# Optimization experiments

Measured on AMD Instinct MI355X. Metric: run time of the kernel, lower is better.

The kernel has to match this reference:

```python
import jax, jax.numpy as jnp
import numpy as np

B, N, DIM = 64, 197, 768
NUM_HEAD, HEAD_DIM = 12, 64
SCALE = HEAD_DIM ** -0.5
WS = (14, 14)
NUM_REL = (2 * WS[0] - 1) * (2 * WS[1] - 1) + 3  # 732


def _relative_position_index():
    coords = np.stack(np.meshgrid(np.arange(WS[0]), np.arange(WS[1]), indexing='ij'))  # (2, Wh, Ww)
    cf = coords.reshape(2, -1)                              # (2, Wh*Ww)
    rel = (cf[:, :, None] - cf[:, None, :]).transpose(1, 2, 0).astype(np.int64)
    rel[:, :, 0] += WS[0] - 1
    rel[:, :, 1] += WS[1] - 1
    rel[:, :, 0] *= 2 * WS[1] - 1
    idx = np.zeros((WS[0] * WS[1] + 1,) * 2, dtype=np.int32)
    idx[1:, 1:] = rel.sum(-1)
    idx[0, :] = NUM_REL - 3
    idx[:, 0] = NUM_REL - 2
    idx[0, 0] = NUM_REL - 1
    return idx


def setup_inputs() -> dict:
    key = jax.random.key(0)
    k1, k2, k3, k4 = jax.random.split(key, 4)
    x = jax.random.normal(k1, (B, N, DIM), dtype=jnp.float32)
    qkv_w = jax.random.normal(k2, (3 * DIM, DIM), dtype=jnp.float32) * (DIM ** -0.5)
    q_bias = jnp.zeros((DIM,), dtype=jnp.float32)
    v_bias = jnp.zeros((DIM,), dtype=jnp.float32)
    rpb_table = jax.random.normal(k3, (NUM_REL, NUM_HEAD), dtype=jnp.float32) * 0.02
    proj_w = jax.random.normal(k4, (DIM, DIM), dtype=jnp.float32) * (DIM ** -0.5)
    proj_b = jnp.zeros((DIM,), dtype=jnp.float32)
    rel_index = jnp.asarray(_relative_position_index())
    return {"x": x, "qkv_w": qkv_w, "q_bias": q_bias, "v_bias": v_bias,
            "rpb_table": rpb_table, "proj_w": proj_w, "proj_b": proj_b,
            "rel_index": rel_index}


def reference(x, qkv_w, q_bias, v_bias, rpb_table, proj_w, proj_b, rel_index):
    b, n, c = x.shape
    # qkv projection with [q_bias, 0, v_bias] bias layout
    qkv_bias = jnp.concatenate([q_bias, jnp.zeros_like(v_bias), v_bias])
    qkv = x @ qkv_w.T + qkv_bias                               # (B, N, 3*C)
    qkv = qkv.reshape(b, n, 3, NUM_HEAD, HEAD_DIM).transpose(2, 0, 3, 1, 4)
    q, k, v = qkv[0] * SCALE, qkv[1], qkv[2]                   # (B, H, N, hd)
    attn = jnp.einsum('bhqd,bhkd->bhqk', q, k)                 # (B, H, N, N)
    # relative position bias gather: table[(N,N)] -> (N, N, H) -> (H, N, N)
    bias = rpb_table[rel_index].transpose(2, 0, 1)
    attn = jax.nn.softmax(attn + bias[None], axis=-1)
    out = jnp.einsum('bhqk,bhkd->bhqd', attn, v)               # (B, H, N, hd)
    out = out.transpose(0, 2, 1, 3).reshape(b, n, -1)
    return out @ proj_w.T + proj_b
```

## Files before the change

### kernel.cpp

```cpp
#include <hip/hip_runtime.h>


#define B_    64
#define N_    197
#define DIM_  768
#define H_    12
#define HD_   64
#define M_TOT (B_ * N_)

#define OFF_Q   0
#define OFF_K   14976
#define OFF_VT  29952
#define ST_A0   44800
#define ST_A1   51456
#define ST_B0   58112
#define ST_B1   64256
#define OFF_P   44800
#define LDS_TOT 74496

typedef __attribute__((ext_vector_type(8))) short bf8;
typedef __attribute__((ext_vector_type(4))) float f4;

__device__ __forceinline__ unsigned short f2bf(float f) {
    unsigned u = __float_as_uint(f);
    u = (u + 0x7fffu + ((u >> 16) & 1u)) >> 16;
    return (unsigned short)u;
}

__device__ __forceinline__ void gl2lds16(const unsigned short* g, unsigned short* l) {
    __builtin_amdgcn_global_load_lds(
        (const __attribute__((address_space(1))) void*)g,
        (__attribute__((address_space(3))) void*)l, 16, 0, 0);
}

__global__ void k_prep(const float* __restrict__ x, const float* __restrict__ qkvw,
                       const float* __restrict__ projw, const float* __restrict__ rpb,
                       const int* __restrict__ relidx,
                       unsigned short* __restrict__ x_bf, unsigned short* __restrict__ qkvw_bf,
                       unsigned short* __restrict__ projw_bf, float* __restrict__ bias_hqk) {
    const int T = gridDim.x * blockDim.x;
    const int tid = blockIdx.x * blockDim.x + threadIdx.x;
    for (int i = tid; i < M_TOT * DIM_; i += T) x_bf[i] = f2bf(x[i]);
    for (int i = tid; i < 3 * DIM_ * DIM_; i += T) qkvw_bf[i] = f2bf(qkvw[i]);
    for (int i = tid; i < DIM_ * DIM_; i += T) projw_bf[i] = f2bf(projw[i]);
    for (int i = tid; i < H_ * N_ * N_; i += T) {
        int h = i / (N_ * N_), qk = i - h * (N_ * N_);
        bias_hqk[i] = rpb[relidx[qk] * H_ + h];
    }
}

__global__ __launch_bounds__(512, 1) void k_fused(const unsigned short* __restrict__ X,
                                                  const unsigned short* __restrict__ Wqkv,
                                                  const float* __restrict__ qb,
                                                  const float* __restrict__ vbias,
                                                  const float* __restrict__ bias_hqk,
                                                  unsigned short* __restrict__ att_ws) {
    __shared__ unsigned short lds[LDS_TOT];

    const int t = threadIdx.x;
    const int w = t >> 6, lane = t & 63, ln = lane & 15, quad = lane >> 4;
    const int wm = w & 3, wn = w >> 2;
    const int srl = lane >> 3;
    const int src8 = (lane & 7) ^ srl;

    const int gid = blockIdx.x;
    const int local = gid >> 3;
    const int b = (gid & 7) * 8 + (local & 7);
    const int h = local >> 3;

    const unsigned short* xb = X + (size_t)b * 197 * 768;

    auto stage = [&](int kt, int aOfs, int bOfs) {
#pragma unroll
        for (int i = 0; i < 4; ++i) {
            int idx = w + 8 * i;
            if (idx >= 25) break;
            if (idx < 13) {
                int tok = 2 * (idx * 8 + srl) + (src8 >> 2);
                if (tok > 196) tok = 196;
                gl2lds16(xb + (size_t)tok * 768 + kt * 32 + (src8 & 3) * 8,
                         &lds[aOfs + idx * 512]);
            } else {
                int bb = idx - 13;
                int rr = 2 * (bb * 8 + srl) + (src8 >> 2);
                gl2lds16(Wqkv + (size_t)((rr >> 6) * 768 + h * 64 + (rr & 63)) * 768
                              + kt * 32 + (src8 & 3) * 8,
                         &lds[bOfs + bb * 512]);
            }
        }
    };

    f4 acc[3][4][2] = {};

    auto compute = [&](int aOfs, int bOfs) {
        bf8 bfr[3][2];
#pragma unroll
        for (int p = 0; p < 3; ++p)
#pragma unroll
            for (int j2 = 0; j2 < 2; ++j2) {
                int rr = p * 64 + (wn * 2 + j2) * 16 + ln;
                int sr = rr >> 1;
                int slot = (((rr & 1) << 2) | quad) ^ (sr & 7);
                bfr[p][j2] = *(const bf8*)&lds[bOfs + sr * 64 + slot * 8];
            }
#pragma unroll
        for (int mi = 0; mi < 4; ++mi) {
            int mt = wm + 4 * mi;
            if (mt >= 13) continue;
            int row = mt * 16 + ln;
            int sr = row >> 1;
            int slot = (((row & 1) << 2) | quad) ^ (sr & 7);
            bf8 af = *(const bf8*)&lds[aOfs + sr * 64 + slot * 8];
#pragma unroll
            for (int p = 0; p < 3; ++p)
#pragma unroll
                for (int j2 = 0; j2 < 2; ++j2)
                    acc[p][mi][j2] = __builtin_amdgcn_mfma_f32_16x16x32_bf16(
                        af, bfr[p][j2], acc[p][mi][j2], 0, 0, 0);
        }
    };

    stage(0, ST_A0, ST_B0);
    for (int kt2 = 0; kt2 < 24; kt2 += 2) {
        __syncthreads();
        if (kt2 + 1 < 24) stage(kt2 + 1, ST_A1, ST_B1);
        compute(ST_A0, ST_B0);
        __syncthreads();
        if (kt2 + 2 < 24) stage(kt2 + 2, ST_A0, ST_B0);
        if (kt2 + 1 < 24) compute(ST_A1, ST_B1);
    }

#pragma unroll
    for (int p = 0; p < 3; ++p) {
        float bj[2];
#pragma unroll
        for (int j2 = 0; j2 < 2; ++j2) {
            int d = h * 64 + (wn * 2 + j2) * 16 + ln;
            bj[j2] = (p == 0) ? qb[d] : (p == 2) ? vbias[d] : 0.0f;
        }
#pragma unroll
        for (int mi = 0; mi < 4; ++mi) {
            int mt = wm + 4 * mi;
            if (mt >= 13) continue;
#pragma unroll
            for (int j2 = 0; j2 < 2; ++j2) {
                int col = (wn * 2 + j2) * 16 + ln;
#pragma unroll
                for (int r = 0; r < 4; ++r) {
                    int row = mt * 16 + quad * 4 + r;
                    float v = acc[p][mi][j2][r];
                    if (p == 0)      lds[OFF_Q + row * 72 + col] = f2bf((v + bj[j2]) * 0.125f);
                    else if (p == 1) lds[OFF_K + row * 72 + col] = f2bf(v);
                    else             lds[OFF_VT + col * 232 + row] = f2bf(v + bj[j2]);
                }
            }
        }
    }
    __syncthreads();

    for (int idx = t; idx < 64 * 16; idx += 512) {
        int row = idx >> 4, c = 208 + (idx & 15);
        lds[OFF_VT + row * 232 + c] = 0;
    }
    __syncthreads();

    const float* bp = bias_hqk + h * 197 * 197;
    unsigned short* psl = &lds[OFF_P + w * 3712];

    for (int mt = w; mt < 13; mt += 8) {
        bf8 qa[2];
#pragma unroll
        for (int ks = 0; ks < 2; ++ks)
            qa[ks] = *(const bf8*)&lds[OFF_Q + (mt * 16 + ln) * 72 + ks * 32 + quad * 8];

        f4 sacc[13];
#pragma unroll
        for (int nt = 0; nt < 13; ++nt) sacc[nt] = (f4){0.f, 0.f, 0.f, 0.f};
#pragma unroll
        for (int nt = 0; nt < 13; ++nt) {
#pragma unroll
            for (int ks = 0; ks < 2; ++ks) {
                bf8 kb = *(const bf8*)&lds[OFF_K + (nt * 16 + ln) * 72 + ks * 32 + quad * 8];
                sacc[nt] = __builtin_amdgcn_mfma_f32_16x16x32_bf16(qa[ks], kb, sacc[nt], 0, 0, 0);
            }
        }

        int qi[4];
#pragma unroll
        for (int r = 0; r < 4; ++r) { int q0 = mt * 16 + quad * 4 + r; qi[r] = q0 < 197 ? q0 : 196; }
        float mx[4] = {-3.0e38f, -3.0e38f, -3.0e38f, -3.0e38f};
#pragma unroll
        for (int nt = 0; nt < 13; ++nt) {
            int kidx = nt * 16 + ln;
#pragma unroll
            for (int r = 0; r < 4; ++r) {
                float s = (kidx < 197) ? (sacc[nt][r] + bp[qi[r] * 197 + kidx]) : -3.0e38f;
                sacc[nt][r] = s;
                mx[r] = fmaxf(mx[r], s);
            }
        }
#pragma unroll
        for (int r = 0; r < 4; ++r)
#pragma unroll
            for (int off = 1; off < 16; off <<= 1)
                mx[r] = fmaxf(mx[r], __shfl_xor(mx[r], off, 64));

        float sum[4] = {0.f, 0.f, 0.f, 0.f};
#pragma unroll
        for (int nt = 0; nt < 13; ++nt)
#pragma unroll
            for (int r = 0; r < 4; ++r) {
                float pv = __expf(sacc[nt][r] - mx[r]);
                sacc[nt][r] = pv;
                sum[r] += pv;
            }
#pragma unroll
        for (int r = 0; r < 4; ++r)
#pragma unroll
            for (int off = 1; off < 16; off <<= 1)
                sum[r] += __shfl_xor(sum[r], off, 64);
        float inv[4];
#pragma unroll
        for (int r = 0; r < 4; ++r) inv[r] = 1.0f / sum[r];

#pragma unroll
        for (int nt = 0; nt < 13; ++nt)
#pragma unroll
            for (int r = 0; r < 4; ++r)
                psl[(quad * 4 + r) * 232 + nt * 16 + ln] = f2bf(sacc[nt][r] * inv[r]);
        for (int i = lane; i < 256; i += 64)
            psl[(i >> 4) * 232 + 208 + (i & 15)] = 0;
        __asm__ __volatile__("s_waitcnt lgkmcnt(0)" ::: "memory");

        bf8 pa[7];
#pragma unroll
        for (int ks = 0; ks < 7; ++ks)
            pa[ks] = *(const bf8*)&psl[ln * 232 + ks * 32 + quad * 8];
#pragma unroll
        for (int j = 0; j < 4; ++j) {
            f4 o = (f4){0.f, 0.f, 0.f, 0.f};
#pragma unroll
            for (int ks = 0; ks < 7; ++ks) {
                bf8 vf = *(const bf8*)&lds[OFF_VT + (j * 16 + ln) * 232 + ks * 32 + quad * 8];
                o = __builtin_amdgcn_mfma_f32_16x16x32_bf16(pa[ks], vf, o, 0, 0, 0);
            }
#pragma unroll
            for (int r = 0; r < 4; ++r) {
                int tok = mt * 16 + quad * 4 + r;
                if (tok < 197)
                    att_ws[((size_t)b * 197 + tok) * 768 + h * 64 + j * 16 + ln] = f2bf(o[r]);
            }
        }
        __asm__ __volatile__("s_waitcnt lgkmcnt(0)" ::: "memory");
    }
}

__device__ __forceinline__ void pj_stage(const unsigned short* __restrict__ A,
                                         const unsigned short* __restrict__ Bm,
                                         int bm, int bn, int kt, int w, int rsub, int src8,
                                         unsigned short* a_l, unsigned short* b_l) {
#pragma unroll
    for (int c = 0; c < 4; ++c) {
        int rb = w * 32 + c * 8;
        int gr = bm * 128 + rb + rsub;
        if (gr > M_TOT - 1) gr = M_TOT - 1;
        gl2lds16(A + (size_t)gr * 768 + kt * 64 + (src8 << 3), &a_l[rb * 64]);
        int gc = bn * 128 + rb + rsub;
        gl2lds16(Bm + (size_t)gc * 768 + kt * 64 + (src8 << 3), &b_l[rb * 64]);
    }
}

__device__ __forceinline__ void pj_compute(const unsigned short* a_l, const unsigned short* b_l,
                                           int wm, int wn, int ln, int quad, f4 (*acc)[4]) {
#pragma unroll
    for (int ks = 0; ks < 2; ++ks) {
        bf8 af[4], bfr[4];
#pragma unroll
        for (int i = 0; i < 4; ++i)
            af[i] = *(const bf8*)&a_l[((wm * 64 + i * 16 + ln) << 6) +
                                      ((((ks << 2) + quad) ^ (ln & 7)) << 3)];
#pragma unroll
        for (int j = 0; j < 4; ++j)
            bfr[j] = *(const bf8*)&b_l[((wn * 64 + j * 16 + ln) << 6) +
                                       ((((ks << 2) + quad) ^ (ln & 7)) << 3)];
#pragma unroll
        for (int i = 0; i < 4; ++i)
#pragma unroll
            for (int j = 0; j < 4; ++j)
                acc[i][j] = __builtin_amdgcn_mfma_f32_16x16x32_bf16(af[i], bfr[j], acc[i][j], 0, 0, 0);
    }
}

__global__ __launch_bounds__(256) void k_proj(const unsigned short* __restrict__ A,
                                              const unsigned short* __restrict__ Bm,
                                              const float* __restrict__ pb,
                                              float* __restrict__ out) {
    __shared__ unsigned short a0[128 * 64], a1[128 * 64];
    __shared__ unsigned short b0[128 * 64], b1[128 * 64];
    const int t = threadIdx.x;
    const int w = t >> 6, lane = t & 63, ln = lane & 15, quad = lane >> 4;
    const int wm = w & 1, wn = w >> 1;

    const int gid = blockIdx.x;
    const int panel = gid / 48, rem = gid - panel * 48;
    const int pm0 = panel * 8;
    const int psz = (99 - pm0 < 8) ? (99 - pm0) : 8;
    const int bm = pm0 + rem % psz;
    const int bn = rem / psz;

    const int rsub = lane >> 3;
    const int src8 = (lane & 7) ^ rsub;

    f4 acc[4][4] = {};

    pj_stage(A, Bm, bm, bn, 0, w, rsub, src8, a0, b0);
#pragma unroll
    for (int kt2 = 0; kt2 < 12; kt2 += 2) {
        __syncthreads();
        if (kt2 + 1 < 12) pj_stage(A, Bm, bm, bn, kt2 + 1, w, rsub, src8, a1, b1);
        pj_compute(a0, b0, wm, wn, ln, quad, acc);
        __syncthreads();
        if (kt2 + 2 < 12) pj_stage(A, Bm, bm, bn, kt2 + 2, w, rsub, src8, a0, b0);
        if (kt2 + 1 < 12) pj_compute(a1, b1, wm, wn, ln, quad, acc);
    }

#pragma unroll
    for (int i = 0; i < 4; ++i) {
#pragma unroll
        for (int r = 0; r < 4; ++r) {
            int row_g = bm * 128 + wm * 64 + i * 16 + quad * 4 + r;
            if (row_g >= M_TOT) continue;
#pragma unroll
            for (int j = 0; j < 4; ++j) {
                int col_g = bn * 128 + wn * 64 + j * 16 + ln;
                out[(size_t)row_g * 768 + col_g] = acc[i][j][r] + pb[col_g];
            }
        }
    }
}

extern "C" void kernel_launch(void* const* d_in, const int* in_sizes, int n_in,
                              void* d_out, int out_size, void* d_ws, size_t ws_size,
                              hipStream_t stream) {
    const float* x     = (const float*)d_in[0];
    const float* qkvw  = (const float*)d_in[1];
    const float* qb    = (const float*)d_in[2];
    const float* vb    = (const float*)d_in[3];
    const float* rpb   = (const float*)d_in[4];
    const float* projw = (const float*)d_in[5];
    const float* pb    = (const float*)d_in[6];
    const int*   ridx  = (const int*)d_in[7];
    float* out = (float*)d_out;

    char* ws = (char*)d_ws;
    size_t off = 0;
    auto alloc = [&](size_t bytes) -> void* {
        void* p = ws + off;
        off = (off + bytes + 255) & ~(size_t)255;
        return p;
    };
    unsigned short* x_bf     = (unsigned short*)alloc((size_t)M_TOT * DIM_ * 2);
    unsigned short* qkvw_bf  = (unsigned short*)alloc((size_t)3 * DIM_ * DIM_ * 2);
    unsigned short* projw_bf = (unsigned short*)alloc((size_t)DIM_ * DIM_ * 2);
    float*          bias_h   = (float*)alloc((size_t)H_ * N_ * N_ * 4);
    unsigned short* att_ws   = (unsigned short*)alloc((size_t)(M_TOT + 64) * DIM_ * 2);
    (void)ws_size; (void)in_sizes; (void)n_in; (void)out_size;

    k_prep<<<1200, 256, 0, stream>>>(x, qkvw, projw, rpb, ridx,
                                     x_bf, qkvw_bf, projw_bf, bias_h);
    k_fused<<<768, 512, 0, stream>>>(x_bf, qkvw_bf, qb, vb, bias_h, att_ws);
    k_proj<<<594, 256, 0, stream>>>(att_ws, projw_bf, pb, out);
}
```

Before: 226.7 us.

## Shrink LDS footprint, keep P in registers via bpermute, raise fused-kernel occupancy

Compacts the fused attention kernel's shared memory by aliasing the GEMM staging buffers with Q/K/V storage and adding XOR-swizzled Q/K/V^T layouts. Computes S^T (K as A operand) so each lane owns one query row, which reduces softmax reductions to two shuffles. The softmax probabilities are repacked in registers with ds_bpermute instead of going through an LDS round trip. The QKV GEMM warp tiling changes from 4x2 to 2x4 with fewer accumulators, launch bounds allow four blocks per CU, and s_setprio is placed around the MFMA loops. The aim is better latency hiding through higher occupancy and less LDS traffic, at the risk of register pressure and extra permute instructions.

New measurement: 433.2 us. 91.1% more time.

```diff
diff --git a/kernel.cpp b/kernel.cpp
--- a/kernel.cpp
+++ b/kernel.cpp
@@ -9,14 +9,13 @@
 #define M_TOT (B_ * N_)
 
 #define OFF_Q   0
-#define OFF_K   14976
-#define OFF_VT  29952
-#define ST_A0   44800
-#define ST_A1   51456
-#define ST_B0   58112
-#define ST_B1   64256
-#define OFF_P   44800
-#define LDS_TOT 74496
+#define OFF_K   13312
+#define OFF_VT  26624
+#define ST_A0   0
+#define ST_A1   6656
+#define ST_B0   13312
+#define ST_B1   19456
+#define LDS_TOT 40960
 
 typedef __attribute__((ext_vector_type(8))) short bf8;
 typedef __attribute__((ext_vector_type(4))) float f4;
@@ -31,6 +30,15 @@
     __builtin_amdgcn_global_load_lds(
         (const __attribute__((address_space(1))) void*)g,
         (__attribute__((address_space(3))) void*)l, 16, 0, 0);
+}
+
+__device__ __forceinline__ int qkaddr(int row, int col) {
+    return row * 64 + ((((col >> 3) ^ row) & 7) << 3) + (col & 7);
+}
+__device__ __forceinline__ int vtaddr(int d, int k) {
+    int s = k >> 3;
+    int s2 = (s < 24) ? ((s & 24) | ((s ^ d) & 7)) : (24 + ((s ^ d) & 3));
+    return d * 224 + (s2 << 3) + (k & 7);
 }
 
 __global__ void k_prep(const float* __restrict__ x, const float* __restrict__ qkvw,
@@ -49,7 +57,7 @@
     }
 }
 
-__global__ __launch_bounds__(512, 1) void k_fused(const unsigned short* __restrict__ X,
+__global__ __launch_bounds__(512, 4) void k_fused(const unsigned short* __restrict__ X,
                                                   const unsigned short* __restrict__ Wqkv,
                                                   const float* __restrict__ qb,
                                                   const float* __restrict__ vbias,
@@ -59,7 +67,7 @@
 
     const int t = threadIdx.x;
     const int w = t >> 6, lane = t & 63, ln = lane & 15, quad = lane >> 4;
-    const int wm = w & 3, wn = w >> 2;
+    const int wm2 = w & 1, wn2 = w >> 1;
     const int srl = lane >> 3;
     const int src8 = (lane & 7) ^ srl;
 
@@ -90,33 +98,29 @@
         }
     };
 
-    f4 acc[3][4][2] = {};
+    f4 acc[7][3] = {};
 
     auto compute = [&](int aOfs, int bOfs) {
-        bf8 bfr[3][2];
-#pragma unroll
-        for (int p = 0; p < 3; ++p)
-#pragma unroll
-            for (int j2 = 0; j2 < 2; ++j2) {
-                int rr = p * 64 + (wn * 2 + j2) * 16 + ln;
-                int sr = rr >> 1;
-                int slot = (((rr & 1) << 2) | quad) ^ (sr & 7);
-                bfr[p][j2] = *(const bf8*)&lds[bOfs + sr * 64 + slot * 8];
-            }
-#pragma unroll
-        for (int mi = 0; mi < 4; ++mi) {
-            int mt = wm + 4 * mi;
+        bf8 bfr[3];
+#pragma unroll
+        for (int tl = 0; tl < 3; ++tl) {
+            int rr = (wn2 * 3 + tl) * 16 + ln;
+            int sr = rr >> 1;
+            int slot = (((rr & 1) << 2) | quad) ^ (sr & 7);
+            bfr[tl] = *(const bf8*)&lds[bOfs + sr * 64 + slot * 8];
+        }
+#pragma unroll
+        for (int mi = 0; mi < 7; ++mi) {
+            int mt = wm2 + 2 * mi;
             if (mt >= 13) continue;
             int row = mt * 16 + ln;
             int sr = row >> 1;
             int slot = (((row & 1) << 2) | quad) ^ (sr & 7);
             bf8 af = *(const bf8*)&lds[aOfs + sr * 64 + slot * 8];
 #pragma unroll
-            for (int p = 0; p < 3; ++p)
-#pragma unroll
-                for (int j2 = 0; j2 < 2; ++j2)
-                    acc[p][mi][j2] = __builtin_amdgcn_mfma_f32_16x16x32_bf16(
-                        af, bfr[p][j2], acc[p][mi][j2], 0, 0, 0);
+            for (int tl = 0; tl < 3; ++tl)
+                acc[mi][tl] = __builtin_amdgcn_mfma_f32_16x16x32_bf16(
+                    af, bfr[tl], acc[mi][tl], 0, 0, 0);
         }
     };
 
@@ -129,129 +133,131 @@
         if (kt2 + 2 < 24) stage(kt2 + 2, ST_A0, ST_B0);
         if (kt2 + 1 < 24) compute(ST_A1, ST_B1);
     }
-
-#pragma unroll
-    for (int p = 0; p < 3; ++p) {
-        float bj[2];
-#pragma unroll
-        for (int j2 = 0; j2 < 2; ++j2) {
-            int d = h * 64 + (wn * 2 + j2) * 16 + ln;
-            bj[j2] = (p == 0) ? qb[d] : (p == 2) ? vbias[d] : 0.0f;
-        }
-#pragma unroll
-        for (int mi = 0; mi < 4; ++mi) {
-            int mt = wm + 4 * mi;
+    __syncthreads();
+
+#pragma unroll
+    for (int tl = 0; tl < 3; ++tl) {
+        int tn = wn2 * 3 + tl;
+        int p = tn >> 2;
+        int col = (tn & 3) * 16 + ln;
+        int d = h * 64 + col;
+        float bj = (p == 0) ? qb[d] : (p == 2) ? vbias[d] : 0.0f;
+#pragma unroll
+        for (int mi = 0; mi < 7; ++mi) {
+            int mt = wm2 + 2 * mi;
             if (mt >= 13) continue;
 #pragma unroll
-            for (int j2 = 0; j2 < 2; ++j2) {
-                int col = (wn * 2 + j2) * 16 + ln;
-#pragma unroll
-                for (int r = 0; r < 4; ++r) {
-                    int row = mt * 16 + quad * 4 + r;
-                    float v = acc[p][mi][j2][r];
-                    if (p == 0)      lds[OFF_Q + row * 72 + col] = f2bf((v + bj[j2]) * 0.125f);
-                    else if (p == 1) lds[OFF_K + row * 72 + col] = f2bf(v);
-                    else             lds[OFF_VT + col * 232 + row] = f2bf(v + bj[j2]);
-                }
-            }
-        }
+            for (int r = 0; r < 4; ++r) {
+                int row = mt * 16 + quad * 4 + r;
+                float v = acc[mi][tl][r];
+                if (p == 0)      lds[OFF_Q + qkaddr(row, col)] = f2bf((v + bj) * 0.125f);
+                else if (p == 1) lds[OFF_K + qkaddr(row, col)] = f2bf(v);
+                else             lds[OFF_VT + vtaddr(col, row)] = f2bf(v + bj);
+            }
+        }
+    }
+    for (int idx = t; idx < 64 * 16; idx += 512) {
+        int d = idx >> 4, k = 208 + (idx & 15);
+        lds[OFF_VT + vtaddr(d, k)] = 0;
     }
     __syncthreads();
 
-    for (int idx = t; idx < 64 * 16; idx += 512) {
-        int row = idx >> 4, c = 208 + (idx & 15);
-        lds[OFF_VT + row * 232 + c] = 0;
-    }
-    __syncthreads();
-
-    const float* bp = bias_hqk + h * 197 * 197;
-    unsigned short* psl = &lds[OFF_P + w * 3712];
+    const float* bp = bias_hqk + (size_t)h * 197 * 197;
 
     for (int mt = w; mt < 13; mt += 8) {
         bf8 qa[2];
 #pragma unroll
         for (int ks = 0; ks < 2; ++ks)
-            qa[ks] = *(const bf8*)&lds[OFF_Q + (mt * 16 + ln) * 72 + ks * 32 + quad * 8];
+            qa[ks] = *(const bf8*)&lds[OFF_Q + qkaddr(mt * 16 + ln, ks * 32 + quad * 8)];
 
         f4 sacc[13];
 #pragma unroll
         for (int nt = 0; nt < 13; ++nt) sacc[nt] = (f4){0.f, 0.f, 0.f, 0.f};
+        __builtin_amdgcn_s_setprio(1);
 #pragma unroll
         for (int nt = 0; nt < 13; ++nt) {
 #pragma unroll
             for (int ks = 0; ks < 2; ++ks) {
-                bf8 kb = *(const bf8*)&lds[OFF_K + (nt * 16 + ln) * 72 + ks * 32 + quad * 8];
-                sacc[nt] = __builtin_amdgcn_mfma_f32_16x16x32_bf16(qa[ks], kb, sacc[nt], 0, 0, 0);
-            }
-        }
-
-        int qi[4];
-#pragma unroll
-        for (int r = 0; r < 4; ++r) { int q0 = mt * 16 + quad * 4 + r; qi[r] = q0 < 197 ? q0 : 196; }
-        float mx[4] = {-3.0e38f, -3.0e38f, -3.0e38f, -3.0e38f};
+                bf8 ka = *(const bf8*)&lds[OFF_K + qkaddr(nt * 16 + ln, ks * 32 + quad * 8)];
+                sacc[nt] = __builtin_amdgcn_mfma_f32_16x16x32_bf16(ka, qa[ks], sacc[nt], 0, 0, 0);
+            }
+        }
+        __builtin_amdgcn_s_setprio(0);
+
+        int qg = mt * 16 + ln;
+        const float* brow = bp + (size_t)(qg < 197 ? qg : 196) * 197;
+        float mx = -3.0e38f;
+#pragma unroll
+        for (int nt = 0; nt < 13; ++nt)
+#pragma unroll
+            for (int r = 0; r < 4; ++r) {
+                int kg = nt * 16 + quad * 4 + r;
+                float s = (kg < 197) ? (sacc[nt][r] + brow[kg]) : -3.0e38f;
+                sacc[nt][r] = s;
+                mx = fmaxf(mx, s);
+            }
+        mx = fmaxf(mx, __shfl_xor(mx, 16, 64));
+        mx = fmaxf(mx, __shfl_xor(mx, 32, 64));
+        float sum = 0.f;
+#pragma unroll
+        for (int nt = 0; nt < 13; ++nt)
+#pragma unroll
+            for (int r = 0; r < 4; ++r) {
+                float pv = __expf(sacc[nt][r] - mx);
+                sacc[nt][r] = pv;
+                sum += pv;
+            }
+        sum += __shfl_xor(sum, 16, 64);
+        sum += __shfl_xor(sum, 32, 64);
+        float inv = 1.0f / sum;
+
+        unsigned pk[14][2];
 #pragma unroll
         for (int nt = 0; nt < 13; ++nt) {
-            int kidx = nt * 16 + ln;
-#pragma unroll
-            for (int r = 0; r < 4; ++r) {
-                float s = (kidx < 197) ? (sacc[nt][r] + bp[qi[r] * 197 + kidx]) : -3.0e38f;
-                sacc[nt][r] = s;
-                mx[r] = fmaxf(mx[r], s);
-            }
-        }
-#pragma unroll
-        for (int r = 0; r < 4; ++r)
-#pragma unroll
-            for (int off = 1; off < 16; off <<= 1)
-                mx[r] = fmaxf(mx[r], __shfl_xor(mx[r], off, 64));
-
-        float sum[4] = {0.f, 0.f, 0.f, 0.f};
-#pragma unroll
-        for (int nt = 0; nt < 13; ++nt)
-#pragma unroll
-            for (int r = 0; r < 4; ++r) {
-                float pv = __expf(sacc[nt][r] - mx[r]);
-                sacc[nt][r] = pv;
-                sum[r] += pv;
-            }
-#pragma unroll
-        for (int r = 0; r < 4; ++r)
-#pragma unroll
-            for (int off = 1; off < 16; off <<= 1)
-                sum[r] += __shfl_xor(sum[r], off, 64);
-        float inv[4];
-#pragma unroll
-        for (int r = 0; r < 4; ++r) inv[r] = 1.0f / sum[r];
-
-#pragma unroll
-        for (int nt = 0; nt < 13; ++nt)
-#pragma unroll
-            for (int r = 0; r < 4; ++r)
-                psl[(quad * 4 + r) * 232 + nt * 16 + ln] = f2bf(sacc[nt][r] * inv[r]);
-        for (int i = lane; i < 256; i += 64)
-            psl[(i >> 4) * 232 + 208 + (i & 15)] = 0;
-        __asm__ __volatile__("s_waitcnt lgkmcnt(0)" ::: "memory");
-
-        bf8 pa[7];
-#pragma unroll
-        for (int ks = 0; ks < 7; ++ks)
-            pa[ks] = *(const bf8*)&psl[ln * 232 + ks * 32 + quad * 8];
-#pragma unroll
-        for (int j = 0; j < 4; ++j) {
-            f4 o = (f4){0.f, 0.f, 0.f, 0.f};
-#pragma unroll
-            for (int ks = 0; ks < 7; ++ks) {
-                bf8 vf = *(const bf8*)&lds[OFF_VT + (j * 16 + ln) * 232 + ks * 32 + quad * 8];
-                o = __builtin_amdgcn_mfma_f32_16x16x32_bf16(pa[ks], vf, o, 0, 0, 0);
-            }
+            pk[nt][0] = (unsigned)f2bf(sacc[nt][0] * inv) |
+                        ((unsigned)f2bf(sacc[nt][1] * inv) << 16);
+            pk[nt][1] = (unsigned)f2bf(sacc[nt][2] * inv) |
+                        ((unsigned)f2bf(sacc[nt][3] * inv) << 16);
+        }
+        pk[13][0] = 0; pk[13][1] = 0;
+
+        const int sA = (((lane & 15) | ((lane & 16) << 1)) << 2);
+        const int sB = sA + 64;
+        const bool hi = (lane & 32) != 0;
+        f4 o[4];
+#pragma unroll
+        for (int j = 0; j < 4; ++j) o[j] = (f4){0.f, 0.f, 0.f, 0.f};
+#pragma unroll
+        for (int ks = 0; ks < 7; ++ks) {
+            int b0 = __builtin_amdgcn_ds_bpermute(sA, (int)pk[2 * ks][0]);
+            int b1 = __builtin_amdgcn_ds_bpermute(sA, (int)pk[2 * ks][1]);
+            int b2 = __builtin_amdgcn_ds_bpermute(sB, (int)pk[2 * ks][0]);
+            int b3 = __builtin_amdgcn_ds_bpermute(sB, (int)pk[2 * ks][1]);
+            int c0 = __builtin_amdgcn_ds_bpermute(sA, (int)pk[2 * ks + 1][0]);
+            int c1 = __builtin_amdgcn_ds_bpermute(sA, (int)pk[2 * ks + 1][1]);
+            int c2 = __builtin_amdgcn_ds_bpermute(sB, (int)pk[2 * ks + 1][0]);
+            int c3 = __builtin_amdgcn_ds_bpermute(sB, (int)pk[2 * ks + 1][1]);
+            union { int u[4]; bf8 v; } uu;
+            uu.u[0] = hi ? c0 : b0;
+            uu.u[1] = hi ? c1 : b1;
+            uu.u[2] = hi ? c2 : b2;
+            uu.u[3] = hi ? c3 : b3;
+            __builtin_amdgcn_s_setprio(1);
+#pragma unroll
+            for (int j = 0; j < 4; ++j) {
+                bf8 vf = *(const bf8*)&lds[OFF_VT + vtaddr(j * 16 + ln, ks * 32 + quad * 8)];
+                o[j] = __builtin_amdgcn_mfma_f32_16x16x32_bf16(uu.v, vf, o[j], 0, 0, 0);
+            }
+            __builtin_amdgcn_s_setprio(0);
+        }
+#pragma unroll
+        for (int j = 0; j < 4; ++j)
 #pragma unroll
             for (int r = 0; r < 4; ++r) {
                 int tok = mt * 16 + quad * 4 + r;
                 if (tok < 197)
-                    att_ws[((size_t)b * 197 + tok) * 768 + h * 64 + j * 16 + ln] = f2bf(o[r]);
-            }
-        }
-        __asm__ __volatile__("s_waitcnt lgkmcnt(0)" ::: "memory");
+                    att_ws[((size_t)b * 197 + tok) * 768 + h * 64 + j * 16 + ln] = f2bf(o[j][r]);
+            }
     }
 }
 
```
